# Performance work log

Measured on AMD Instinct MI355X. Metric: run time of the kernel, lower is better.

Reference implementation:

```python
import jax, jax.numpy as jnp
import numpy as np

B, N, C, D, H = 256, 1024, 100, 256, 16
QD = D // H              # per-head dim
CLIP = 10.0              # logit_clipping
NEG = -1000000000.0      # masked_fill value in torch source


def setup_inputs() -> dict:
    key = jax.random.key(0)
    ks = jax.random.split(key, 12)
    s = 0.05
    inp = {
        "depot_embedding": jax.random.normal(ks[0], (B, 1, D), jnp.float32),
        "cluster_embedding": jax.random.normal(ks[1], (B, C + 1, D), jnp.float32),
        "current_embedding": jax.random.normal(ks[2], (B, 1, D), jnp.float32),
        "node_embeddings": jax.random.normal(ks[3], (B, N, D), jnp.float32),
        # visited-node / other-cluster / visited-cluster masks (bool)
        "mask": jax.random.bernoulli(ks[4], 0.2, (B, 1, N)),
        "cluster_mask": jax.random.bernoulli(ks[5], 0.5, (B, 1, N)),
        "visited_cluster_mask": jax.random.bernoulli(ks[6], 0.3, (B, 1, C + 1)).at[:, :, C].set(False),
        # Linear weights stored as (in, out) so y = x @ W
        "Wq": jax.random.normal(ks[7], (3 * D, D), jnp.float32) * s,
        "Wk": jax.random.normal(ks[8], (D, D), jnp.float32) * s,
        "Wv": jax.random.normal(ks[9], (D, D), jnp.float32) * s,
        "Wks": jax.random.normal(ks[10], (D, D), jnp.float32) * s,
        "Wo": jax.random.normal(ks[11], (D, D), jnp.float32) * s,
    }
    return inp


def _unvisited_mean(emb, m):
    # emb: [B,N,D], m: [B,1,N] bool -> masked mean over unvisited nodes [B,1,D]
    keep = (~m).astype(emb.dtype).transpose(0, 2, 1)          # [B,N,1]
    denom = jnp.clip(keep.sum(axis=1, keepdims=True), 1.0)    # [B,1,1]
    return (emb * keep).sum(axis=1, keepdims=True) / denom


def reference(depot_embedding, cluster_embedding, current_embedding,
              node_embeddings, mask, cluster_mask, visited_cluster_mask,
              Wq, Wk, Wv, Wks, Wo):
    b = node_embeddings.shape[0]
    # context query: [unvisited-mean, current, depot] -> [B,1,3D]
    uv = _unvisited_mean(node_embeddings, mask)
    context = jnp.concatenate([uv, current_embedding, depot_embedding], axis=-1)
    q = context @ Wq                    # [B,1,D]
    k = cluster_embedding @ Wk          # [B,C+1,D]
    v = cluster_embedding @ Wv
    prob_k = cluster_embedding @ Wks

    # visited-cluster mask; depot (col 0) only allowed once all real clusters visited
    vm = visited_cluster_mask[:, 0, :]                        # [B,C+1]
    all_real_visited = jnp.all(vm[:, 1:], axis=1)
    vm = vm.at[:, 0].set(~all_real_visited)

    # multi-head glimpse attention
    qh = q.reshape(b, 1, H, QD).transpose(0, 2, 1, 3)         # [B,H,1,QD]
    kh = k.reshape(b, -1, H, QD).transpose(0, 2, 1, 3)        # [B,H,C+1,QD]
    vh = v.reshape(b, -1, H, QD).transpose(0, 2, 1, 3)
    scores = jnp.einsum('bhqe,bhke->bhqk', qh, kh) / jnp.sqrt(jnp.float32(QD))
    scores = jnp.where(vm[:, None, None, :], NEG, scores)
    attn = jax.nn.softmax(scores, axis=-1)
    glimpse = jnp.einsum('bhqk,bhke->bhqe', attn, vh)
    glimpse = glimpse.transpose(0, 2, 1, 3).reshape(b, 1, D) @ Wo   # [B,1,D]

    # single-head pointer logits over clusters
    logits = jnp.einsum('bqd,bkd->bqk', glimpse, prob_k)[:, 0, :] / jnp.sqrt(jnp.float32(D))
    logits = jnp.tanh(logits) * CLIP
    logits = jnp.where(vm, NEG, logits)
    local_log_p = jax.nn.log_softmax(logits, axis=1)          # [B,C+1]

    # greedy cluster selection + gather
    selected_cluster = jnp.argmax(local_log_p, axis=1)        # [B] int
    sel_emb = jnp.take_along_axis(cluster_embedding,
                                  selected_cluster[:, None, None], axis=1)  # [B,1,D]

    uvc = _unvisited_mean(node_embeddings, mask | cluster_mask)
    init_aug = jnp.concatenate([uvc, current_embedding, sel_emb, depot_embedding], axis=-1)  # [B,1,4D]
    init_guidance_emb = sel_emb
    init_guidance = selected_cluster
    clu_prob = local_log_p
    return init_aug, init_guidance_emb, init_guidance, clu_prob
```

## Files before the change

### kernel.cpp

```cpp
#include <hip/hip_runtime.h>
#include <math.h>

#define B_SZ 256
#define N_SZ 1024
#define NCL  101
#define D_SZ 256
#define NH   16
#define APAD 260
#define NEGV (-1000000000.0f)


__device__ __forceinline__ bool mask_at(const void* p, long idx, int mode) {
  if (mode == 0) return ((const int*)p)[idx] != 0;
  if (mode == 1) return ((const unsigned char*)p)[idx] != 0;
  return ((const float*)p)[idx] != 0.0f;
}

__global__ void detect_mode_kernel(const unsigned int* m, int* flag) {
  if (threadIdx.x == 0 && blockIdx.x == 0) {
    bool isf = false, nonbin = false;
    for (int i = 0; i < 256; ++i) {
      unsigned int v = m[i];
      if (v == 0x3F800000u) isf = true;
      else if (v > 1u) nonbin = true;
    }
    *flag = isf ? 2 : (nonbin ? 1 : 0);
  }
}

__global__ __launch_bounds__(512) void mean_kernel(
    const float* __restrict__ node, const void* __restrict__ mask,
    const void* __restrict__ cmask, const int* __restrict__ flag,
    float* __restrict__ uv, float* __restrict__ uvc) {
  const int b = blockIdx.x, tid = threadIdx.x;
  const int mode = *flag;
  __shared__ float f1[N_SZ], f2[N_SZ];
  __shared__ int wcnt1[8], wcnt2[8];
  __shared__ float red[8][D_SZ];

  int c1 = 0, c2 = 0;
  for (int n = tid; n < N_SZ; n += 512) {
    const bool m1 = mask_at(mask,  (long)b * N_SZ + n, mode);
    const bool m2 = mask_at(cmask, (long)b * N_SZ + n, mode);
    const int k1 = m1 ? 0 : 1;
    const int k2 = (m1 || m2) ? 0 : 1;
    f1[n] = (float)k1; f2[n] = (float)k2;
    c1 += k1; c2 += k2;
  }
  for (int off = 32; off > 0; off >>= 1) {
    c1 += __shfl_down(c1, off);
    c2 += __shfl_down(c2, off);
  }
  if ((tid & 63) == 0) { wcnt1[tid >> 6] = c1; wcnt2[tid >> 6] = c2; }
  __syncthreads();
  int t1 = 0, t2 = 0;
  #pragma unroll
  for (int w = 0; w < 8; ++w) { t1 += wcnt1[w]; t2 += wcnt2[w]; }
  const float den1 = fmaxf((float)t1, 1.0f);
  const float den2 = fmaxf((float)t2, 1.0f);

  const int rg = tid >> 6;
  const int c4 = (tid & 63) << 2;
  const float* base = node + (size_t)b * N_SZ * D_SZ + c4;
  float4 s1 = {0.f,0.f,0.f,0.f}, s2 = {0.f,0.f,0.f,0.f};
  for (int n = rg; n < N_SZ; n += 8) {
    const float4 x = *(const float4*)(base + (size_t)n * D_SZ);
    const float k1 = f1[n], k2 = f2[n];
    s1.x = fmaf(x.x, k1, s1.x); s1.y = fmaf(x.y, k1, s1.y);
    s1.z = fmaf(x.z, k1, s1.z); s1.w = fmaf(x.w, k1, s1.w);
    s2.x = fmaf(x.x, k2, s2.x); s2.y = fmaf(x.y, k2, s2.y);
    s2.z = fmaf(x.z, k2, s2.z); s2.w = fmaf(x.w, k2, s2.w);
  }
  *(float4*)&red[rg][c4] = s1;
  __syncthreads();
  if (tid < D_SZ) {
    float t = 0.f;
    #pragma unroll
    for (int r = 0; r < 8; ++r) t += red[r][tid];
    uv[b * D_SZ + tid] = t / den1;
  }
  __syncthreads();
  *(float4*)&red[rg][c4] = s2;
  __syncthreads();
  if (tid < D_SZ) {
    float t = 0.f;
    #pragma unroll
    for (int r = 0; r < 8; ++r) t += red[r][tid];
    uvc[b * D_SZ + tid] = t / den2;
  }
}

struct __align__(16) SMem {
  float At[16][APAD];
  union { float tT[NH][APAD]; float uB[NH][APAD]; } tu;
  float sc[NH][104];
  float ctx[3 * D_SZ];
  float q[D_SZ];
  float g[D_SZ];
  float go[D_SZ];
  float w[D_SZ];
  float logits[104];
  int   vm[104];
  float lse_s;
  int   sel_s;
};

__global__ __launch_bounds__(256) void main_kernel(
    const float* __restrict__ depot, const float* __restrict__ cluster,
    const float* __restrict__ current, const void* __restrict__ vcm,
    const int* __restrict__ flag,
    const float* __restrict__ Wq, const float* __restrict__ Wk,
    const float* __restrict__ Wv, const float* __restrict__ Wks,
    const float* __restrict__ Wo,
    const float* __restrict__ uv, const float* __restrict__ uvc,
    float* __restrict__ out) {
  __shared__ SMem S;
  const int b = blockIdx.x, tid = threadIdx.x;
  const int mode = *flag;
  const float* Ab = cluster + (size_t)b * NCL * D_SZ;

  if (tid < NCL) S.vm[tid] = mask_at(vcm, (long)b * NCL + tid, mode) ? 1 : 0;
  S.ctx[tid]       = uv[b * D_SZ + tid];
  S.ctx[256 + tid] = current[b * D_SZ + tid];
  S.ctx[512 + tid] = depot[b * D_SZ + tid];
  __syncthreads();
  if (tid == 0) {
    int all1 = 1;
    for (int c = 1; c < NCL; ++c) all1 &= S.vm[c];
    S.vm[0] = all1 ? 0 : 1;
  }

  {
    float a0 = 0.f, a1 = 0.f, a2 = 0.f, a3 = 0.f;
    for (int i = 0; i < 3 * D_SZ; i += 4) {
      a0 = fmaf(S.ctx[i + 0], Wq[(size_t)(i + 0) * D_SZ + tid], a0);
      a1 = fmaf(S.ctx[i + 1], Wq[(size_t)(i + 1) * D_SZ + tid], a1);
      a2 = fmaf(S.ctx[i + 2], Wq[(size_t)(i + 2) * D_SZ + tid], a2);
      a3 = fmaf(S.ctx[i + 3], Wq[(size_t)(i + 3) * D_SZ + tid], a3);
    }
    S.q[tid] = (a0 + a1) + (a2 + a3);
  }
  __syncthreads();

  {
    const int h = tid & 15, i0 = tid >> 4;
    float qh[16];
    #pragma unroll
    for (int e = 0; e < 16; ++e) qh[e] = S.q[h * 16 + e];
    for (int k = 0; k < 16; ++k) {
      const int i = i0 + 16 * k;
      const float* wr = Wk + (size_t)i * D_SZ + h * 16;
      float acc = 0.f;
      #pragma unroll
      for (int e = 0; e < 16; ++e) acc = fmaf(wr[e], qh[e], acc);
      S.tu.tT[h][i] = acc;
    }
  }
  __syncthreads();

  for (int ch = 0; ch < 7; ++ch) {
    const int r0 = ch * 16;
    for (int x = tid; x < 16 * 64; x += 256) {
      const int r = x >> 6, cc = (x & 63) << 2;
      if (r0 + r < NCL) {
        const float4 v = *(const float4*)(Ab + (size_t)(r0 + r) * D_SZ + cc);
        *(float4*)&S.At[r][cc] = v;
      }
    }
    __syncthreads();
    {
      const int h = tid >> 4, cl = tid & 15, c = r0 + cl;
      float p0 = 0.f, p1 = 0.f, p2 = 0.f, p3 = 0.f;
      for (int i = 0; i < D_SZ; i += 4) {
        const float4 av = *(const float4*)&S.At[cl][i];
        const float4 tv = *(const float4*)&S.tu.tT[h][i];
        p0 = fmaf(av.x, tv.x, p0);
        p1 = fmaf(av.y, tv.y, p1);
        p2 = fmaf(av.z, tv.z, p2);
        p3 = fmaf(av.w, tv.w, p3);
      }
      if (c < NCL) {
        float sv = 0.25f * ((p0 + p1) + (p2 + p3));
        if (S.vm[c]) sv = NEGV;
        S.sc[h][c] = sv;
      }
    }
    __syncthreads();
  }

  {
    const int h = tid >> 4, j = tid & 15;
    float m = -3.0e38f;
    for (int c = j; c < NCL; c += 16) m = fmaxf(m, S.sc[h][c]);
    #pragma unroll
    for (int off = 8; off > 0; off >>= 1) m = fmaxf(m, __shfl_xor(m, off, 16));
    float ssum = 0.f;
    for (int c = j; c < NCL; c += 16) {
      const float e = expf(S.sc[h][c] - m);
      S.sc[h][c] = e;
      ssum += e;
    }
    #pragma unroll
    for (int off = 8; off > 0; off >>= 1) ssum += __shfl_xor(ssum, off, 16);
    const float inv = 1.0f / ssum;
    for (int c = j; c < NCL; c += 16) S.sc[h][c] *= inv;
  }
  __syncthreads();

  {
    float u[16];
    #pragma unroll
    for (int h = 0; h < 16; ++h) u[h] = 0.f;
    for (int ch = 0; ch < 7; ++ch) {
      const int r0 = ch * 16;
      for (int x = tid; x < 16 * 64; x += 256) {
        const int r = x >> 6, cc = (x & 63) << 2;
        if (r0 + r < NCL) {
          const float4 v = *(const float4*)(Ab + (size_t)(r0 + r) * D_SZ + cc);
          *(float4*)&S.At[r][cc] = v;
        }
      }
      __syncthreads();
      const int cmax = (NCL - r0 < 16) ? (NCL - r0) : 16;
      for (int cl = 0; cl < cmax; ++cl) {
        const float a = S.At[cl][tid];
        const int c = r0 + cl;
        #pragma unroll
        for (int h = 0; h < 16; ++h) u[h] = fmaf(S.sc[h][c], a, u[h]);
      }
      __syncthreads();
    }
    #pragma unroll
    for (int h = 0; h < 16; ++h) S.tu.uB[h][tid] = u[h];
  }
  __syncthreads();

  {
    const int h = tid >> 4;
    float p0 = 0.f, p1 = 0.f, p2 = 0.f, p3 = 0.f;
    for (int i = 0; i < D_SZ; i += 4) {
      p0 = fmaf(S.tu.uB[h][i + 0], Wv[(size_t)(i + 0) * D_SZ + tid], p0);
      p1 = fmaf(S.tu.uB[h][i + 1], Wv[(size_t)(i + 1) * D_SZ + tid], p1);
      p2 = fmaf(S.tu.uB[h][i + 2], Wv[(size_t)(i + 2) * D_SZ + tid], p2);
      p3 = fmaf(S.tu.uB[h][i + 3], Wv[(size_t)(i + 3) * D_SZ + tid], p3);
    }
    S.g[tid] = (p0 + p1) + (p2 + p3);
  }
  __syncthreads();

  {
    float p0 = 0.f, p1 = 0.f, p2 = 0.f, p3 = 0.f;
    for (int d = 0; d < D_SZ; d += 4) {
      p0 = fmaf(S.g[d + 0], Wo[(size_t)(d + 0) * D_SZ + tid], p0);
      p1 = fmaf(S.g[d + 1], Wo[(size_t)(d + 1) * D_SZ + tid], p1);
      p2 = fmaf(S.g[d + 2], Wo[(size_t)(d + 2) * D_SZ + tid], p2);
      p3 = fmaf(S.g[d + 3], Wo[(size_t)(d + 3) * D_SZ + tid], p3);
    }
    S.go[tid] = (p0 + p1) + (p2 + p3);
  }
  __syncthreads();

  {
    const float* wr = Wks + (size_t)tid * D_SZ;
    float p0 = 0.f, p1 = 0.f, p2 = 0.f, p3 = 0.f;
    for (int j = 0; j < D_SZ; j += 4) {
      const float4 w4 = *(const float4*)&wr[j];
      p0 = fmaf(w4.x, S.go[j + 0], p0);
      p1 = fmaf(w4.y, S.go[j + 1], p1);
      p2 = fmaf(w4.z, S.go[j + 2], p2);
      p3 = fmaf(w4.w, S.go[j + 3], p3);
    }
    S.w[tid] = (p0 + p1) + (p2 + p3);
  }
  __syncthreads();

  if (tid < NCL) {
    const float* ar = Ab + (size_t)tid * D_SZ;
    float p0 = 0.f, p1 = 0.f, p2 = 0.f, p3 = 0.f;
    for (int i = 0; i < D_SZ; i += 4) {
      const float4 a4 = *(const float4*)&ar[i];
      p0 = fmaf(a4.x, S.w[i + 0], p0);
      p1 = fmaf(a4.y, S.w[i + 1], p1);
      p2 = fmaf(a4.z, S.w[i + 2], p2);
      p3 = fmaf(a4.w, S.w[i + 3], p3);
    }
    float l = ((p0 + p1) + (p2 + p3)) * 0.0625f;
    l = tanhf(l) * 10.0f;
    if (S.vm[tid]) l = NEGV;
    S.logits[tid] = l;
  }
  __syncthreads();

  if (tid < 64) {
    float bv = -3.0e38f; int bi = 0;
    for (int c = tid; c < NCL; c += 64) {
      const float v = S.logits[c];
      if (v > bv) { bv = v; bi = c; }
    }
    #pragma unroll
    for (int off = 32; off > 0; off >>= 1) {
      const float ov = __shfl_xor(bv, off);
      const int   oi = __shfl_xor(bi, off);
      if (ov > bv || (ov == bv && oi < bi)) { bv = ov; bi = oi; }
    }
    float ss = 0.f;
    for (int c = tid; c < NCL; c += 64) ss += expf(S.logits[c] - bv);
    #pragma unroll
    for (int off = 32; off > 0; off >>= 1) ss += __shfl_xor(ss, off);
    if (tid == 0) { S.lse_s = bv + logf(ss); S.sel_s = bi; }
  }
  __syncthreads();

  const float lse = S.lse_s;
  const int sel = S.sel_s;
  if (tid < NCL) out[327936 + b * NCL + tid] = S.logits[tid] - lse;
  if (tid == 0)  out[327680 + b] = (float)sel;
  const float se = Ab[(size_t)sel * D_SZ + tid];
  out[262144 + b * D_SZ + tid] = se;
  float* ia = out + (size_t)b * 1024;
  ia[tid]       = uvc[b * D_SZ + tid];
  ia[256 + tid] = current[b * D_SZ + tid];
  ia[512 + tid] = se;
  ia[768 + tid] = depot[b * D_SZ + tid];
}

extern "C" void kernel_launch(void* const* d_in, const int* in_sizes, int n_in,
                              void* d_out, int out_size, void* d_ws, size_t ws_size,
                              hipStream_t stream) {
  const float* depot   = (const float*)d_in[0];
  const float* cluster = (const float*)d_in[1];
  const float* current = (const float*)d_in[2];
  const float* node    = (const float*)d_in[3];
  const void*  mask    = d_in[4];
  const void*  cmask   = d_in[5];
  const void*  vcm     = d_in[6];
  const float* Wq  = (const float*)d_in[7];
  const float* Wk  = (const float*)d_in[8];
  const float* Wv  = (const float*)d_in[9];
  const float* Wks = (const float*)d_in[10];
  const float* Wo  = (const float*)d_in[11];
  float* out = (float*)d_out;

  int*   flag = (int*)d_ws;
  float* uv   = (float*)((char*)d_ws + 1024);
  float* uvc  = (float*)((char*)d_ws + 1024 + (size_t)B_SZ * D_SZ * 4);

  hipLaunchKernelGGL(detect_mode_kernel, dim3(1), dim3(64), 0, stream,
                     (const unsigned int*)mask, flag);
  hipLaunchKernelGGL(mean_kernel, dim3(B_SZ), dim3(512), 0, stream,
                     node, mask, cmask, flag, uv, uvc);
  hipLaunchKernelGGL(main_kernel, dim3(B_SZ), dim3(256), 0, stream,
                     depot, cluster, current, vcm, flag,
                     Wq, Wk, Wv, Wks, Wo, uv, uvc, out);
}
```

Baseline: 513.1 us.

## Split masked-mean reduction across 8 row-slices per batch with partial sums

Result: faster. 499.3 us (-2.7%).

```diff
diff --git a/kernel.cpp b/kernel.cpp
--- a/kernel.cpp
+++ b/kernel.cpp
@@ -28,44 +28,51 @@
   }
 }
 
-__global__ __launch_bounds__(512) void mean_kernel(
+__global__ __launch_bounds__(256) void mean_partial_kernel(
     const float* __restrict__ node, const void* __restrict__ mask,
     const void* __restrict__ cmask, const int* __restrict__ flag,
-    float* __restrict__ uv, float* __restrict__ uvc) {
-  const int b = blockIdx.x, tid = threadIdx.x;
+    int* __restrict__ counts, float* __restrict__ partials) {
+  const int bs = blockIdx.x;
+  const int b = bs >> 3, s = bs & 7;
+  const int tid = threadIdx.x;
   const int mode = *flag;
-  __shared__ float f1[N_SZ], f2[N_SZ];
-  __shared__ int wcnt1[8], wcnt2[8];
-  __shared__ float red[8][D_SZ];
+  const int r0 = s * 128;
+  __shared__ float f1[128], f2[128];
+  __shared__ int wc1[2], wc2[2];
+  __shared__ float red[4][D_SZ];
 
   int c1 = 0, c2 = 0;
-  for (int n = tid; n < N_SZ; n += 512) {
-    const bool m1 = mask_at(mask,  (long)b * N_SZ + n, mode);
-    const bool m2 = mask_at(cmask, (long)b * N_SZ + n, mode);
+  if (tid < 128) {
+    const long idx = (long)b * N_SZ + r0 + tid;
+    const bool m1 = mask_at(mask, idx, mode);
+    const bool m2 = mask_at(cmask, idx, mode);
     const int k1 = m1 ? 0 : 1;
     const int k2 = (m1 || m2) ? 0 : 1;
-    f1[n] = (float)k1; f2[n] = (float)k2;
-    c1 += k1; c2 += k2;
-  }
+    f1[tid] = (float)k1; f2[tid] = (float)k2;
+    c1 = k1; c2 = k2;
+  }
+  #pragma unroll
   for (int off = 32; off > 0; off >>= 1) {
     c1 += __shfl_down(c1, off);
     c2 += __shfl_down(c2, off);
   }
-  if ((tid & 63) == 0) { wcnt1[tid >> 6] = c1; wcnt2[tid >> 6] = c2; }
-  __syncthreads();
-  int t1 = 0, t2 = 0;
-  #pragma unroll
-  for (int w = 0; w < 8; ++w) { t1 += wcnt1[w]; t2 += wcnt2[w]; }
-  const float den1 = fmaxf((float)t1, 1.0f);
-  const float den2 = fmaxf((float)t2, 1.0f);
+  if (tid == 0)  { wc1[0] = c1; wc2[0] = c2; }
+  if (tid == 64) { wc1[1] = c1; wc2[1] = c2; }
+  __syncthreads();
+  if (tid == 0) {
+    counts[bs * 2 + 0] = wc1[0] + wc1[1];
+    counts[bs * 2 + 1] = wc2[0] + wc2[1];
+  }
 
   const int rg = tid >> 6;
   const int c4 = (tid & 63) << 2;
-  const float* base = node + (size_t)b * N_SZ * D_SZ + c4;
+  const float* base = node + ((size_t)b * N_SZ + r0) * D_SZ + c4;
   float4 s1 = {0.f,0.f,0.f,0.f}, s2 = {0.f,0.f,0.f,0.f};
-  for (int n = rg; n < N_SZ; n += 8) {
-    const float4 x = *(const float4*)(base + (size_t)n * D_SZ);
-    const float k1 = f1[n], k2 = f2[n];
+  #pragma unroll 8
+  for (int k = 0; k < 32; ++k) {
+    const int row = rg * 32 + k;
+    const float4 x = *(const float4*)(base + (size_t)row * D_SZ);
+    const float k1 = f1[row], k2 = f2[row];
     s1.x = fmaf(x.x, k1, s1.x); s1.y = fmaf(x.y, k1, s1.y);
     s1.z = fmaf(x.z, k1, s1.z); s1.w = fmaf(x.w, k1, s1.w);
     s2.x = fmaf(x.x, k2, s2.x); s2.y = fmaf(x.y, k2, s2.y);
@@ -73,20 +80,16 @@
   }
   *(float4*)&red[rg][c4] = s1;
   __syncthreads();
-  if (tid < D_SZ) {
-    float t = 0.f;
-    #pragma unroll
-    for (int r = 0; r < 8; ++r) t += red[r][tid];
-    uv[b * D_SZ + tid] = t / den1;
+  {
+    float t = red[0][tid] + red[1][tid] + red[2][tid] + red[3][tid];
+    partials[((size_t)bs * 2 + 0) * D_SZ + tid] = t;
   }
   __syncthreads();
   *(float4*)&red[rg][c4] = s2;
   __syncthreads();
-  if (tid < D_SZ) {
-    float t = 0.f;
-    #pragma unroll
-    for (int r = 0; r < 8; ++r) t += red[r][tid];
-    uvc[b * D_SZ + tid] = t / den2;
+  {
+    float t = red[0][tid] + red[1][tid] + red[2][tid] + red[3][tid];
+    partials[((size_t)bs * 2 + 1) * D_SZ + tid] = t;
   }
 }
 
@@ -112,15 +115,29 @@
     const float* __restrict__ Wq, const float* __restrict__ Wk,
     const float* __restrict__ Wv, const float* __restrict__ Wks,
     const float* __restrict__ Wo,
-    const float* __restrict__ uv, const float* __restrict__ uvc,
+    const int* __restrict__ counts, const float* __restrict__ partials,
     float* __restrict__ out) {
   __shared__ SMem S;
   const int b = blockIdx.x, tid = threadIdx.x;
   const int mode = *flag;
   const float* Ab = cluster + (size_t)b * NCL * D_SZ;
 
+  float uvv = 0.f, uvcv = 0.f;
+  #pragma unroll
+  for (int s = 0; s < 8; ++s) {
+    uvv  += partials[((size_t)(b * 8 + s) * 2 + 0) * D_SZ + tid];
+    uvcv += partials[((size_t)(b * 8 + s) * 2 + 1) * D_SZ + tid];
+  }
+  int t1 = 0, t2 = 0;
+  #pragma unroll
+  for (int s = 0; s < 8; ++s) {
+    t1 += counts[(b * 8 + s) * 2 + 0];
+    t2 += counts[(b * 8 + s) * 2 + 1];
+  }
+  const float uvcval = uvcv / fmaxf((float)t2, 1.0f);
+
   if (tid < NCL) S.vm[tid] = mask_at(vcm, (long)b * NCL + tid, mode) ? 1 : 0;
-  S.ctx[tid]       = uv[b * D_SZ + tid];
+  S.ctx[tid]       = uvv / fmaxf((float)t1, 1.0f);
   S.ctx[256 + tid] = current[b * D_SZ + tid];
   S.ctx[512 + tid] = depot[b * D_SZ + tid];
   __syncthreads();
@@ -318,7 +335,7 @@
   const float se = Ab[(size_t)sel * D_SZ + tid];
   out[262144 + b * D_SZ + tid] = se;
   float* ia = out + (size_t)b * 1024;
-  ia[tid]       = uvc[b * D_SZ + tid];
+  ia[tid]       = uvcval;
   ia[256 + tid] = current[b * D_SZ + tid];
   ia[512 + tid] = se;
   ia[768 + tid] = depot[b * D_SZ + tid];
@@ -341,15 +358,15 @@
   const float* Wo  = (const float*)d_in[11];
   float* out = (float*)d_out;
 
-  int*   flag = (int*)d_ws;
-  float* uv   = (float*)((char*)d_ws + 1024);
-  float* uvc  = (float*)((char*)d_ws + 1024 + (size_t)B_SZ * D_SZ * 4);
+  int*   flag     = (int*)d_ws;
+  int*   counts   = (int*)((char*)d_ws + 1024);
+  float* partials = (float*)((char*)d_ws + 1024 + 16384);
 
   hipLaunchKernelGGL(detect_mode_kernel, dim3(1), dim3(64), 0, stream,
                      (const unsigned int*)mask, flag);
-  hipLaunchKernelGGL(mean_kernel, dim3(B_SZ), dim3(512), 0, stream,
-                     node, mask, cmask, flag, uv, uvc);
+  hipLaunchKernelGGL(mean_partial_kernel, dim3(B_SZ * 8), dim3(256), 0, stream,
+                     node, mask, cmask, flag, counts, partials);
   hipLaunchKernelGGL(main_kernel, dim3(B_SZ), dim3(256), 0, stream,
                      depot, cluster, current, vcm, flag,
-                     Wq, Wk, Wv, Wks, Wo, uv, uvc, out);
-}
+                     Wq, Wk, Wv, Wks, Wo, counts, partials, out);
+}
```
